# Kernel tuning notes

Hardware: AMD Instinct MI355X
Metric: run time of the kernel (lower is better)

Reference implementation:

```python
import jax, jax.numpy as jnp
import numpy as np

N_NODES = 100000
DIM = 64
N_EDGES = 1250000
PRESERVE = 0.1  # preserve_ratio in GCN module


def gcn_conv(x, W, b, row, col, edge_w, num_nodes):
    """PyG GCNConv with normalize=True: symmetric norm with added self-loops.
    x: [N, d], W: [d, d_out], edge (row -> col) with weight edge_w: [E].
    """
    # add self-loops with weight 1
    loop = jnp.arange(num_nodes, dtype=row.dtype)
    r = jnp.concatenate([row, loop])
    c = jnp.concatenate([col, loop])
    w = jnp.concatenate([edge_w, jnp.ones((num_nodes,), dtype=edge_w.dtype)])
    # symmetric degree normalization: deg computed at target (col)
    deg = jax.ops.segment_sum(w, c, num_segments=num_nodes)
    dinv = jnp.where(deg > 0, jax.lax.rsqrt(deg), 0.0)
    norm = dinv[r] * w * dinv[c]  # [E+N]
    xw = x @ W  # [N, d_out] (linear transform before propagation)
    msg = xw[r] * norm[:, None]  # gather + scale
    out = jax.ops.segment_sum(msg, c, num_segments=num_nodes)  # scatter-add at targets
    return out + b


def setup_inputs() -> dict:
    key = jax.random.key(0)
    ks = jax.random.split(key, 8)
    skill_embed = jax.random.normal(ks[0], (N_NODES, DIM), dtype=jnp.float32)
    edge_index = jax.random.randint(ks[1], (2, N_EDGES), 0, N_NODES, dtype=jnp.int64)
    edge_attr = jax.random.uniform(ks[2], (N_EDGES,), dtype=jnp.float32)
    # GCNConv params (W stored as [in, out] here), glorot-ish init
    scale = 1.0 / np.sqrt(DIM)
    W1 = jax.random.uniform(ks[3], (DIM, DIM), minval=-scale, maxval=scale, dtype=jnp.float32)
    b1 = jnp.zeros((DIM,), dtype=jnp.float32)
    W2 = jax.random.uniform(ks[4], (DIM, DIM), minval=-scale, maxval=scale, dtype=jnp.float32)
    b2 = jnp.zeros((DIM,), dtype=jnp.float32)
    return {"skill_embed": skill_embed, "edge_index": edge_index, "edge_attr": edge_attr,
            "W1": W1, "b1": b1, "W2": W2, "b2": b2}


def reference(skill_embed, edge_index, edge_attr, W1, b1, W2, b2):
    row, col = edge_index[0], edge_index[1]
    n = skill_embed.shape[0]
    temp = skill_embed
    out = gcn_conv(skill_embed, W1, b1, row, col, edge_attr, n)
    temp = (1.0 - PRESERVE) * out + PRESERVE * temp
    out = gcn_conv(temp, W2, b2, row, col, edge_attr, n)
    temp = (1.0 - PRESERVE) * out + PRESERVE * temp
    return temp
```

## Files before the change

### kernel.cpp

```cpp
#include <hip/hip_runtime.h>

#define DIM 64
#define PRESERVE 0.1f

typedef unsigned short bf16_t;

__device__ __forceinline__ float readlane_f(float v, int l) {
    return __int_as_float(__builtin_amdgcn_readlane(__float_as_int(v), l));
}
__device__ __forceinline__ float bf2f(bf16_t u) {
    return __uint_as_float(((unsigned)u) << 16);
}
__device__ __forceinline__ bf16_t f2bf(float f) {
    unsigned u = __float_as_uint(f);
    unsigned r = (u + 0x7FFFu + ((u >> 16) & 1u)) >> 16;
    return (bf16_t)r;
}

__global__ void k_init(int* cursor, int n) {
    int i = blockIdx.x * blockDim.x + threadIdx.x;
    if (i < n) cursor[i] = 0;
}

__global__ void k_hist4(const int4* __restrict__ col4, int* cursor,
                        int4* __restrict__ rank4, int nthreads) {
    int t = blockIdx.x * blockDim.x + threadIdx.x;
    if (t >= nthreads) return;
    int4 c = col4[t];
    int4 r;
    r.x = atomicAdd(&cursor[c.x], 1);
    r.y = atomicAdd(&cursor[c.y], 1);
    r.z = atomicAdd(&cursor[c.z], 1);
    r.w = atomicAdd(&cursor[c.w], 1);
    rank4[t] = r;
}

__global__ void k_hist1(const int* __restrict__ col, int* cursor,
                        int* __restrict__ rank, int E) {
    int e = blockIdx.x * blockDim.x + threadIdx.x;
    if (e < E) rank[e] = atomicAdd(&cursor[col[e]], 1);
}

__global__ __launch_bounds__(256) void k_scan1(const int* __restrict__ counts,
                                               int* __restrict__ offsets,
                                               int* __restrict__ blksum, int n) {
    __shared__ int s[256];
    int t = threadIdx.x;
    int idx = blockIdx.x * 256 + t;
    int v = (idx < n) ? counts[idx] : 0;
    s[t] = v;
    __syncthreads();
    for (int off = 1; off < 256; off <<= 1) {
        int x = (t >= off) ? s[t - off] : 0;
        __syncthreads();
        s[t] += x;
        __syncthreads();
    }
    if (idx < n) offsets[idx] = s[t];
    if (t == 255) blksum[blockIdx.x] = s[255];
}

__global__ __launch_bounds__(512) void k_scan2(const int* __restrict__ blksum,
                                               int* __restrict__ blkoff, int nblk) {
    __shared__ int s[512];
    int t = threadIdx.x;
    int v = (t < nblk) ? blksum[t] : 0;
    s[t] = v;
    __syncthreads();
    for (int off = 1; off < 512; off <<= 1) {
        int x = (t >= off) ? s[t - off] : 0;
        __syncthreads();
        s[t] += x;
        __syncthreads();
    }
    if (t < nblk) blkoff[t] = s[t] - v;
}

__global__ __launch_bounds__(256) void k_scan3(const int* __restrict__ counts,
                                               int* __restrict__ offsets,
                                               const int* __restrict__ blkoff,
                                               int n, int E) {
    int t = threadIdx.x;
    int idx = blockIdx.x * 256 + t;
    if (idx < n) offsets[idx] = offsets[idx] - counts[idx] + blkoff[blockIdx.x];
    if (idx == 0) offsets[n] = E;
}

__global__ void k_fill4(const int4* __restrict__ row4, const int4* __restrict__ col4,
                        const float4* __restrict__ w4, const int4* __restrict__ rank4,
                        const int* __restrict__ offsets, int2* __restrict__ sedge,
                        int nthreads) {
    int t = blockIdx.x * blockDim.x + threadIdx.x;
    if (t >= nthreads) return;
    int4 r = row4[t];
    int4 c = col4[t];
    float4 w = w4[t];
    int4 k = rank4[t];
    int2 p;
    p.x = r.x; p.y = __float_as_int(w.x); sedge[offsets[c.x] + k.x] = p;
    p.x = r.y; p.y = __float_as_int(w.y); sedge[offsets[c.y] + k.y] = p;
    p.x = r.z; p.y = __float_as_int(w.z); sedge[offsets[c.z] + k.z] = p;
    p.x = r.w; p.y = __float_as_int(w.w); sedge[offsets[c.w] + k.w] = p;
}

__global__ void k_fill1(const int* __restrict__ row, const int* __restrict__ col,
                        const float* __restrict__ w, const int* __restrict__ rank,
                        const int* __restrict__ offsets, int2* __restrict__ sedge,
                        int E) {
    int e = blockIdx.x * blockDim.x + threadIdx.x;
    if (e >= E) return;
    int2 p;
    p.x = row[e];
    p.y = __float_as_int(w[e]);
    sedge[offsets[col[e]] + rank[e]] = p;
}

__global__ __launch_bounds__(256) void k_deg_seg(const int2* __restrict__ sedge,
                                                 const int* __restrict__ offsets,
                                                 float* __restrict__ dinv, int n) {
    int tid = threadIdx.x;
    int lane = tid & 63;
    int c = blockIdx.x * 4 + (tid >> 6);
    if (c >= n) return;
    int beg = offsets[c];
    int end = offsets[c + 1];
    float s = 0.0f;
    for (int j = beg + lane; j < end; j += 64) s += __int_as_float(sedge[j].y);
    for (int off = 32; off > 0; off >>= 1) s += __shfl_xor(s, off);
    if (lane == 0) {
        float d = 1.0f + s;
        dinv[c] = (d > 0.0f) ? rsqrtf(d) : 0.0f;
    }
}

__global__ __launch_bounds__(256) void k_mm(
        const float* __restrict__ x, const float* __restrict__ W,
        const float* __restrict__ dinv, bf16_t* __restrict__ xs, int n) {
    int tid = threadIdx.x;
    int lane = tid & 63;
    int waveId = blockIdx.x * 4 + (tid >> 6);
    int nWaves = gridDim.x * 4;

    float Wr[DIM];
#pragma unroll
    for (int k = 0; k < DIM; ++k) Wr[k] = W[k * DIM + lane];

    for (int r0 = waveId * 4; r0 < n; r0 += nWaves * 4) {
        if (r0 + 3 < n) {
            float x0 = x[(size_t)(r0 + 0) * DIM + lane];
            float x1 = x[(size_t)(r0 + 1) * DIM + lane];
            float x2 = x[(size_t)(r0 + 2) * DIM + lane];
            float x3 = x[(size_t)(r0 + 3) * DIM + lane];
            float a0 = 0.f, a1 = 0.f, a2 = 0.f, a3 = 0.f;
#pragma unroll
            for (int k = 0; k < DIM; ++k) {
                float w = Wr[k];
                a0 += readlane_f(x0, k) * w;
                a1 += readlane_f(x1, k) * w;
                a2 += readlane_f(x2, k) * w;
                a3 += readlane_f(x3, k) * w;
            }
            xs[(size_t)(r0 + 0) * DIM + lane] = f2bf(a0 * dinv[r0 + 0]);
            xs[(size_t)(r0 + 1) * DIM + lane] = f2bf(a1 * dinv[r0 + 1]);
            xs[(size_t)(r0 + 2) * DIM + lane] = f2bf(a2 * dinv[r0 + 2]);
            xs[(size_t)(r0 + 3) * DIM + lane] = f2bf(a3 * dinv[r0 + 3]);
        } else {
            for (int r = r0; r < n; ++r) {
                float xv = x[(size_t)r * DIM + lane];
                float a = 0.f;
#pragma unroll
                for (int k = 0; k < DIM; ++k) a += readlane_f(xv, k) * Wr[k];
                xs[(size_t)r * DIM + lane] = f2bf(a * dinv[r]);
            }
        }
    }
}

__global__ __launch_bounds__(256) void k_gather(
        const bf16_t* __restrict__ xs, const int* __restrict__ offsets,
        const int2* __restrict__ sedge, const float* __restrict__ dinv,
        const float* __restrict__ b, const float* __restrict__ xprev,
        float* __restrict__ out, int n) {
    int tid = threadIdx.x;
    int lane = tid & 63;
    int c = blockIdx.x * 4 + (tid >> 6);
    if (c >= n) return;
    float di = dinv[c];
    float acc = bf2f(xs[(size_t)c * DIM + lane]);
    int beg = offsets[c];
    int end = offsets[c + 1];
    for (int b0 = beg; b0 < end; b0 += 64) {
        int m = end - b0;
        if (m > 64) m = 64;
        int r_l = 0, w_l = 0;
        if (lane < m) {
            int2 p = sedge[b0 + lane];
            r_l = p.x;
            w_l = p.y;
        }
        int j = 0;
        for (; j + 3 < m; j += 4) {
            int r0 = __builtin_amdgcn_readlane(r_l, j);
            int r1 = __builtin_amdgcn_readlane(r_l, j + 1);
            int r2 = __builtin_amdgcn_readlane(r_l, j + 2);
            int r3 = __builtin_amdgcn_readlane(r_l, j + 3);
            float w0 = readlane_f(__int_as_float(w_l), j);
            float w1 = readlane_f(__int_as_float(w_l), j + 1);
            float w2 = readlane_f(__int_as_float(w_l), j + 2);
            float w3 = readlane_f(__int_as_float(w_l), j + 3);
            float a0 = bf2f(xs[(size_t)r0 * DIM + lane]);
            float a1 = bf2f(xs[(size_t)r1 * DIM + lane]);
            float a2 = bf2f(xs[(size_t)r2 * DIM + lane]);
            float a3 = bf2f(xs[(size_t)r3 * DIM + lane]);
            acc += a0 * w0;
            acc += a1 * w1;
            acc += a2 * w2;
            acc += a3 * w3;
        }
        for (; j < m; ++j) {
            int r0 = __builtin_amdgcn_readlane(r_l, j);
            float w0 = readlane_f(__int_as_float(w_l), j);
            acc += bf2f(xs[(size_t)r0 * DIM + lane]) * w0;
        }
    }
    float v = (1.0f - PRESERVE) * (acc * di + b[lane]) + PRESERVE * xprev[(size_t)c * DIM + lane];
    out[(size_t)c * DIM + lane] = v;
}

extern "C" void kernel_launch(void* const* d_in, const int* in_sizes, int n_in,
                              void* d_out, int out_size, void* d_ws, size_t ws_size,
                              hipStream_t stream) {
    const float* x  = (const float*)d_in[0];
    const int*   ei = (const int*)d_in[1];
    const float* ew = (const float*)d_in[2];
    const float* W1 = (const float*)d_in[3];
    const float* b1 = (const float*)d_in[4];
    const float* W2 = (const float*)d_in[5];
    const float* b2 = (const float*)d_in[6];

    const int N = in_sizes[0] / DIM;
    const int E = in_sizes[2];
    const int* row = ei;
    const int* col = ei + E;

    int2* sedge   = (int2*)d_ws;
    float* dinv   = (float*)(sedge + E);
    float* temp   = dinv + N;
    bf16_t* xs    = (bf16_t*)(temp + (size_t)N * DIM);
    int* rank     = (int*)(xs + (size_t)N * DIM);
    int* cursor   = rank + E;
    int* offsets  = cursor + N;
    int* blksum   = offsets + N + 1;
    int* blkoff   = blksum + 640;

    const int B = 256;
    const int nblkN = (N + B - 1) / B;
    const int nblkG = (N + 3) / 4;
    const int nblkMM = 1024;

    k_init<<<nblkN, B, 0, stream>>>(cursor, N);

    if ((E & 3) == 0) {
        int nt = E / 4;
        k_hist4<<<(nt + B - 1) / B, B, 0, stream>>>((const int4*)col, cursor, (int4*)rank, nt);
    } else {
        k_hist1<<<(E + B - 1) / B, B, 0, stream>>>(col, cursor, rank, E);
    }

    k_scan1<<<nblkN, B, 0, stream>>>(cursor, offsets, blksum, N);
    k_scan2<<<1, 512, 0, stream>>>(blksum, blkoff, nblkN);
    k_scan3<<<nblkN, B, 0, stream>>>(cursor, offsets, blkoff, N, E);

    if ((E & 3) == 0) {
        int nt = E / 4;
        k_fill4<<<(nt + B - 1) / B, B, 0, stream>>>((const int4*)row, (const int4*)col,
                                                    (const float4*)ew, (const int4*)rank,
                                                    offsets, sedge, nt);
    } else {
        k_fill1<<<(E + B - 1) / B, B, 0, stream>>>(row, col, ew, rank, offsets, sedge, E);
    }

    k_deg_seg<<<nblkG, B, 0, stream>>>(sedge, offsets, dinv, N);

    k_mm<<<nblkMM, B, 0, stream>>>(x, W1, dinv, xs, N);
    k_gather<<<nblkG, B, 0, stream>>>(xs, offsets, sedge, dinv, b1, x, temp, N);

    k_mm<<<nblkMM, B, 0, stream>>>(temp, W2, dinv, xs, N);
    k_gather<<<nblkG, B, 0, stream>>>(xs, offsets, sedge, dinv, b2, temp, (float*)d_out, N);
}
```

Before: 333.0 us.

## Fuse first matmul into histogram kernel and second matmul into first gather

The first X·W1 transform no longer depends on dinv, so it runs inside the histogram launch, with one third of the blocks doing atomics and the rest doing the matmul. The source-side dinv factor is folded into the edge weights by a new rescale pass. The second matmul is fused into the first gather's epilogue through a persistent-wave loop, removing a separate launch and a round trip of temp. The cost is one extra pass over the edges and a fixed 1/3 block split that may leave work unbalanced. xs2 shares memory with rank, which is only safe because rank is no longer needed by the time xs2 is written.

```diff
diff --git a/kernel.cpp b/kernel.cpp
--- a/kernel.cpp
+++ b/kernel.cpp
@@ -22,23 +22,71 @@
     if (i < n) cursor[i] = 0;
 }
 
-__global__ void k_hist4(const int4* __restrict__ col4, int* cursor,
-                        int4* __restrict__ rank4, int nthreads) {
-    int t = blockIdx.x * blockDim.x + threadIdx.x;
-    if (t >= nthreads) return;
-    int4 c = col4[t];
-    int4 r;
-    r.x = atomicAdd(&cursor[c.x], 1);
-    r.y = atomicAdd(&cursor[c.y], 1);
-    r.z = atomicAdd(&cursor[c.z], 1);
-    r.w = atomicAdd(&cursor[c.w], 1);
-    rank4[t] = r;
-}
-
-__global__ void k_hist1(const int* __restrict__ col, int* cursor,
-                        int* __restrict__ rank, int E) {
-    int e = blockIdx.x * blockDim.x + threadIdx.x;
-    if (e < E) rank[e] = atomicAdd(&cursor[col[e]], 1);
+__global__ __launch_bounds__(256) void k_hist_mm(
+        const int* __restrict__ col, int* __restrict__ cursor,
+        int* __restrict__ rank, int E,
+        const float* __restrict__ x, const float* __restrict__ W,
+        bf16_t* __restrict__ xs, int n) {
+    int bid = blockIdx.x;
+    int G = gridDim.x;
+    if (bid % 3 == 0) {
+        int hb = bid / 3;
+        int nhb = (G + 2) / 3;
+        int tid0 = hb * 256 + threadIdx.x;
+        int nthreads = nhb * 256;
+        int nvec = E >> 2;
+        const int4* col4 = (const int4*)col;
+        int4* rank4 = (int4*)rank;
+        for (int t = tid0; t < nvec; t += nthreads) {
+            int4 c = col4[t];
+            int4 r;
+            r.x = atomicAdd(&cursor[c.x], 1);
+            r.y = atomicAdd(&cursor[c.y], 1);
+            r.z = atomicAdd(&cursor[c.z], 1);
+            r.w = atomicAdd(&cursor[c.w], 1);
+            rank4[t] = r;
+        }
+        for (int e = (nvec << 2) + tid0; e < E; e += nthreads)
+            rank[e] = atomicAdd(&cursor[col[e]], 1);
+    } else {
+        int mb = bid - (bid / 3) - 1;
+        int nmb = G - (G + 2) / 3;
+        int lane = threadIdx.x & 63;
+        int waveId = mb * 4 + (threadIdx.x >> 6);
+        int nWaves = nmb * 4;
+        float Wr[DIM];
+#pragma unroll
+        for (int k = 0; k < DIM; ++k) Wr[k] = W[k * DIM + lane];
+        for (int r0 = waveId * 4; r0 < n; r0 += nWaves * 4) {
+            if (r0 + 3 < n) {
+                float x0 = x[(size_t)(r0 + 0) * DIM + lane];
+                float x1 = x[(size_t)(r0 + 1) * DIM + lane];
+                float x2 = x[(size_t)(r0 + 2) * DIM + lane];
+                float x3 = x[(size_t)(r0 + 3) * DIM + lane];
+                float a0 = 0.f, a1 = 0.f, a2 = 0.f, a3 = 0.f;
+#pragma unroll
+                for (int k = 0; k < DIM; ++k) {
+                    float w = Wr[k];
+                    a0 += readlane_f(x0, k) * w;
+                    a1 += readlane_f(x1, k) * w;
+                    a2 += readlane_f(x2, k) * w;
+                    a3 += readlane_f(x3, k) * w;
+                }
+                xs[(size_t)(r0 + 0) * DIM + lane] = f2bf(a0);
+                xs[(size_t)(r0 + 1) * DIM + lane] = f2bf(a1);
+                xs[(size_t)(r0 + 2) * DIM + lane] = f2bf(a2);
+                xs[(size_t)(r0 + 3) * DIM + lane] = f2bf(a3);
+            } else {
+                for (int r = r0; r < n; ++r) {
+                    float xv = x[(size_t)r * DIM + lane];
+                    float a = 0.f;
+#pragma unroll
+                    for (int k = 0; k < DIM; ++k) a += readlane_f(xv, k) * Wr[k];
+                    xs[(size_t)r * DIM + lane] = f2bf(a);
+                }
+            }
+        }
+    }
 }
 
 __global__ __launch_bounds__(256) void k_scan1(const int* __restrict__ counts,
@@ -133,60 +181,83 @@
     }
 }
 
-__global__ __launch_bounds__(256) void k_mm(
-        const float* __restrict__ x, const float* __restrict__ W,
-        const float* __restrict__ dinv, bf16_t* __restrict__ xs, int n) {
-    int tid = threadIdx.x;
-    int lane = tid & 63;
-    int waveId = blockIdx.x * 4 + (tid >> 6);
+__global__ void k_rescale(int2* sedge, const float* __restrict__ dinv, int E) {
+    int e = blockIdx.x * blockDim.x + threadIdx.x;
+    if (e >= E) return;
+    int2 p = sedge[e];
+    p.y = __float_as_int(__int_as_float(p.y) * dinv[p.x]);
+    sedge[e] = p;
+}
+
+__global__ __launch_bounds__(256) void k_gather_mm(
+        const bf16_t* __restrict__ xs1, const int* __restrict__ offsets,
+        const int2* __restrict__ sedge, const float* __restrict__ dinv,
+        const float* __restrict__ b, const float* __restrict__ xprev,
+        const float* __restrict__ W2, float* __restrict__ temp,
+        bf16_t* __restrict__ xs2, int n) {
+    int lane = threadIdx.x & 63;
+    int waveId = blockIdx.x * 4 + (threadIdx.x >> 6);
     int nWaves = gridDim.x * 4;
 
-    float Wr[DIM];
-#pragma unroll
-    for (int k = 0; k < DIM; ++k) Wr[k] = W[k * DIM + lane];
-
-    for (int r0 = waveId * 4; r0 < n; r0 += nWaves * 4) {
-        if (r0 + 3 < n) {
-            float x0 = x[(size_t)(r0 + 0) * DIM + lane];
-            float x1 = x[(size_t)(r0 + 1) * DIM + lane];
-            float x2 = x[(size_t)(r0 + 2) * DIM + lane];
-            float x3 = x[(size_t)(r0 + 3) * DIM + lane];
-            float a0 = 0.f, a1 = 0.f, a2 = 0.f, a3 = 0.f;
-#pragma unroll
-            for (int k = 0; k < DIM; ++k) {
-                float w = Wr[k];
-                a0 += readlane_f(x0, k) * w;
-                a1 += readlane_f(x1, k) * w;
-                a2 += readlane_f(x2, k) * w;
-                a3 += readlane_f(x3, k) * w;
+    float W2r[DIM];
+#pragma unroll
+    for (int k = 0; k < DIM; ++k) W2r[k] = W2[k * DIM + lane];
+
+    for (int c = waveId; c < n; c += nWaves) {
+        float di = dinv[c];
+        float acc = di * bf2f(xs1[(size_t)c * DIM + lane]);
+        int beg = offsets[c];
+        int end = offsets[c + 1];
+        for (int b0 = beg; b0 < end; b0 += 64) {
+            int m = end - b0;
+            if (m > 64) m = 64;
+            int r_l = 0, w_l = 0;
+            if (lane < m) {
+                int2 p = sedge[b0 + lane];
+                r_l = p.x;
+                w_l = p.y;
             }
-            xs[(size_t)(r0 + 0) * DIM + lane] = f2bf(a0 * dinv[r0 + 0]);
-            xs[(size_t)(r0 + 1) * DIM + lane] = f2bf(a1 * dinv[r0 + 1]);
-            xs[(size_t)(r0 + 2) * DIM + lane] = f2bf(a2 * dinv[r0 + 2]);
-            xs[(size_t)(r0 + 3) * DIM + lane] = f2bf(a3 * dinv[r0 + 3]);
-        } else {
-            for (int r = r0; r < n; ++r) {
-                float xv = x[(size_t)r * DIM + lane];
-                float a = 0.f;
-#pragma unroll
-                for (int k = 0; k < DIM; ++k) a += readlane_f(xv, k) * Wr[k];
-                xs[(size_t)r * DIM + lane] = f2bf(a * dinv[r]);
+            int j = 0;
+            for (; j + 3 < m; j += 4) {
+                int r0 = __builtin_amdgcn_readlane(r_l, j);
+                int r1 = __builtin_amdgcn_readlane(r_l, j + 1);
+                int r2 = __builtin_amdgcn_readlane(r_l, j + 2);
+                int r3 = __builtin_amdgcn_readlane(r_l, j + 3);
+                float w0 = readlane_f(__int_as_float(w_l), j);
+                float w1 = readlane_f(__int_as_float(w_l), j + 1);
+                float w2 = readlane_f(__int_as_float(w_l), j + 2);
+                float w3 = readlane_f(__int_as_float(w_l), j + 3);
+                acc += bf2f(xs1[(size_t)r0 * DIM + lane]) * w0;
+                acc += bf2f(xs1[(size_t)r1 * DIM + lane]) * w1;
+                acc += bf2f(xs1[(size_t)r2 * DIM + lane]) * w2;
+                acc += bf2f(xs1[(size_t)r3 * DIM + lane]) * w3;
             }
-        }
-    }
-}
-
-__global__ __launch_bounds__(256) void k_gather(
-        const bf16_t* __restrict__ xs, const int* __restrict__ offsets,
+            for (; j < m; ++j) {
+                int r0 = __builtin_amdgcn_readlane(r_l, j);
+                float w0 = readlane_f(__int_as_float(w_l), j);
+                acc += bf2f(xs1[(size_t)r0 * DIM + lane]) * w0;
+            }
+        }
+        float tv = (1.0f - PRESERVE) * (acc * di + b[lane])
+                 + PRESERVE * xprev[(size_t)c * DIM + lane];
+        temp[(size_t)c * DIM + lane] = tv;
+        float a = 0.f;
+#pragma unroll
+        for (int k = 0; k < DIM; ++k) a += readlane_f(tv, k) * W2r[k];
+        xs2[(size_t)c * DIM + lane] = f2bf(a);
+    }
+}
+
+__global__ __launch_bounds__(256) void k_gather2(
+        const bf16_t* __restrict__ xs2, const int* __restrict__ offsets,
         const int2* __restrict__ sedge, const float* __restrict__ dinv,
         const float* __restrict__ b, const float* __restrict__ xprev,
         float* __restrict__ out, int n) {
-    int tid = threadIdx.x;
-    int lane = tid & 63;
-    int c = blockIdx.x * 4 + (tid >> 6);
+    int lane = threadIdx.x & 63;
+    int c = blockIdx.x * 4 + (threadIdx.x >> 6);
     if (c >= n) return;
     float di = dinv[c];
-    float acc = bf2f(xs[(size_t)c * DIM + lane]);
+    float acc = di * bf2f(xs2[(size_t)c * DIM + lane]);
     int beg = offsets[c];
     int end = offsets[c + 1];
     for (int b0 = beg; b0 < end; b0 += 64) {
@@ -208,22 +279,19 @@
             float w1 = readlane_f(__int_as_float(w_l), j + 1);
             float w2 = readlane_f(__int_as_float(w_l), j + 2);
             float w3 = readlane_f(__int_as_float(w_l), j + 3);
-            float a0 = bf2f(xs[(size_t)r0 * DIM + lane]);
-            float a1 = bf2f(xs[(size_t)r1 * DIM + lane]);
-            float a2 = bf2f(xs[(size_t)r2 * DIM + lane]);
-            float a3 = bf2f(xs[(size_t)r3 * DIM + lane]);
-            acc += a0 * w0;
-            acc += a1 * w1;
-            acc += a2 * w2;
-            acc += a3 * w3;
+            acc += bf2f(xs2[(size_t)r0 * DIM + lane]) * w0;
+            acc += bf2f(xs2[(size_t)r1 * DIM + lane]) * w1;
+            acc += bf2f(xs2[(size_t)r2 * DIM + lane]) * w2;
+            acc += bf2f(xs2[(size_t)r3 * DIM + lane]) * w3;
         }
         for (; j < m; ++j) {
             int r0 = __builtin_amdgcn_readlane(r_l, j);
             float w0 = readlane_f(__int_as_float(w_l), j);
-            acc += bf2f(xs[(size_t)r0 * DIM + lane]) * w0;
-        }
-    }
-    float v = (1.0f - PRESERVE) * (acc * di + b[lane]) + PRESERVE * xprev[(size_t)c * DIM + lane];
+            acc += bf2f(xs2[(size_t)r0 * DIM + lane]) * w0;
+        }
+    }
+    float v = (1.0f - PRESERVE) * (acc * di + b[lane])
+            + PRESERVE * xprev[(size_t)c * DIM + lane];
     out[(size_t)c * DIM + lane] = v;
 }
 
@@ -246,26 +314,23 @@
     int2* sedge   = (int2*)d_ws;
     float* dinv   = (float*)(sedge + E);
     float* temp   = dinv + N;
-    bf16_t* xs    = (bf16_t*)(temp + (size_t)N * DIM);
-    int* rank     = (int*)(xs + (size_t)N * DIM);
+    bf16_t* xs1   = (bf16_t*)(temp + (size_t)N * DIM);
+    bf16_t* xs2   = xs1 + (size_t)N * DIM;
+    int* rank     = (int*)xs2;
     int* cursor   = rank + E;
-    int* offsets  = cursor + N;
+    int* offsets  = (int*)(xs2 + (size_t)N * DIM);
     int* blksum   = offsets + N + 1;
     int* blkoff   = blksum + 640;
 
     const int B = 256;
     const int nblkN = (N + B - 1) / B;
     const int nblkG = (N + 3) / 4;
-    const int nblkMM = 1024;
+    const int G2 = 1536;
+    const int nblkGM = 1024;
 
     k_init<<<nblkN, B, 0, stream>>>(cursor, N);
 
-    if ((E & 3) == 0) {
-        int nt = E / 4;
-        k_hist4<<<(nt + B - 1) / B, B, 0, stream>>>((const int4*)col, cursor, (int4*)rank, nt);
-    } else {
-        k_hist1<<<(E + B - 1) / B, B, 0, stream>>>(col, cursor, rank, E);
-    }
+    k_hist_mm<<<G2, B, 0, stream>>>(col, cursor, rank, E, x, W1, xs1, N);
 
     k_scan1<<<nblkN, B, 0, stream>>>(cursor, offsets, blksum, N);
     k_scan2<<<1, 512, 0, stream>>>(blksum, blkoff, nblkN);
@@ -281,10 +346,10 @@
     }
 
     k_deg_seg<<<nblkG, B, 0, stream>>>(sedge, offsets, dinv, N);
-
-    k_mm<<<nblkMM, B, 0, stream>>>(x, W1, dinv, xs, N);
-    k_gather<<<nblkG, B, 0, stream>>>(xs, offsets, sedge, dinv, b1, x, temp, N);
-
-    k_mm<<<nblkMM, B, 0, stream>>>(temp, W2, dinv, xs, N);
-    k_gather<<<nblkG, B, 0, stream>>>(xs, offsets, sedge, dinv, b2, temp, (float*)d_out, N);
-}
+    k_rescale<<<(E + B - 1) / B, B, 0, stream>>>(sedge, dinv, E);
+
+    k_gather_mm<<<nblkGM, B, 0, stream>>>(xs1, offsets, sedge, dinv, b1, x,
+                                          W2, temp, xs2, N);
+    k_gather2<<<nblkG, B, 0, stream>>>(xs2, offsets, sedge, dinv, b2, temp,
+                                       (float*)d_out, N);
+}
```

Result: slower. 345.9 us (+3.9%).

## Overlap histogram with first matmul, use decoupled-lookback scan, fuse degree scaling

Applied to the files above, without the earlier changes.

The edge-target histogram and the first layer's x@W1 now run in one kernel, with a third of the blocks doing atomics and the rest doing the matmul, so the atomic-bound and compute-bound work share the machine. The three-pass scan is replaced by a single-pass chunked scan that chains chunks through per-chunk status flags, and the cursor clear becomes a memset. Degree normalisation scaling and the bf16 conversion of the first layer's features are fused into the degree kernel. This removes several launches but adds a spin-wait between scan blocks and an extra full-precision intermediate write and read.

```diff
diff --git a/kernel.cpp b/kernel.cpp
--- a/kernel.cpp
+++ b/kernel.cpp
@@ -2,6 +2,7 @@
 
 #define DIM 64
 #define PRESERVE 0.1f
+#define SCHUNK 1024
 
 typedef unsigned short bf16_t;
 
@@ -17,73 +18,134 @@
     return (bf16_t)r;
 }
 
-__global__ void k_init(int* cursor, int n) {
-    int i = blockIdx.x * blockDim.x + threadIdx.x;
-    if (i < n) cursor[i] = 0;
-}
-
-__global__ void k_hist4(const int4* __restrict__ col4, int* cursor,
-                        int4* __restrict__ rank4, int nthreads) {
-    int t = blockIdx.x * blockDim.x + threadIdx.x;
-    if (t >= nthreads) return;
-    int4 c = col4[t];
-    int4 r;
-    r.x = atomicAdd(&cursor[c.x], 1);
-    r.y = atomicAdd(&cursor[c.y], 1);
-    r.z = atomicAdd(&cursor[c.z], 1);
-    r.w = atomicAdd(&cursor[c.w], 1);
-    rank4[t] = r;
-}
-
-__global__ void k_hist1(const int* __restrict__ col, int* cursor,
-                        int* __restrict__ rank, int E) {
-    int e = blockIdx.x * blockDim.x + threadIdx.x;
-    if (e < E) rank[e] = atomicAdd(&cursor[col[e]], 1);
-}
-
-__global__ __launch_bounds__(256) void k_scan1(const int* __restrict__ counts,
-                                               int* __restrict__ offsets,
-                                               int* __restrict__ blksum, int n) {
+__global__ __launch_bounds__(256) void k_hist_mm(
+        const int* __restrict__ col, int* __restrict__ cursor,
+        int* __restrict__ rank, int E,
+        const float* __restrict__ x, const float* __restrict__ W,
+        float* __restrict__ temp, int n) {
+    const int G = gridDim.x;
+    const int Gh = G / 3;
+    const int bid = blockIdx.x;
+    const int tid = threadIdx.x;
+    if (bid < Gh) {
+        int t0 = bid * 256 + tid;
+        int nh = Gh * 256;
+        int nvec = E >> 2;
+        const int4* col4 = (const int4*)col;
+        int4* rank4 = (int4*)rank;
+        for (int t = t0; t < nvec; t += nh) {
+            int4 c = col4[t];
+            int4 r;
+            r.x = atomicAdd(&cursor[c.x], 1);
+            r.y = atomicAdd(&cursor[c.y], 1);
+            r.z = atomicAdd(&cursor[c.z], 1);
+            r.w = atomicAdd(&cursor[c.w], 1);
+            rank4[t] = r;
+        }
+        for (int e = (nvec << 2) + t0; e < E; e += nh)
+            rank[e] = atomicAdd(&cursor[col[e]], 1);
+    } else {
+        int mb = bid - Gh;
+        int nmb = G - Gh;
+        int lane = tid & 63;
+        int waveId = mb * 4 + (tid >> 6);
+        int nWaves = nmb * 4;
+        float Wr[DIM];
+#pragma unroll
+        for (int k = 0; k < DIM; ++k) Wr[k] = W[k * DIM + lane];
+        for (int r0 = waveId * 4; r0 < n; r0 += nWaves * 4) {
+            if (r0 + 3 < n) {
+                float x0 = x[(size_t)(r0 + 0) * DIM + lane];
+                float x1 = x[(size_t)(r0 + 1) * DIM + lane];
+                float x2 = x[(size_t)(r0 + 2) * DIM + lane];
+                float x3 = x[(size_t)(r0 + 3) * DIM + lane];
+                float a0 = 0.f, a1 = 0.f, a2 = 0.f, a3 = 0.f;
+#pragma unroll
+                for (int k = 0; k < DIM; ++k) {
+                    float w = Wr[k];
+                    a0 += readlane_f(x0, k) * w;
+                    a1 += readlane_f(x1, k) * w;
+                    a2 += readlane_f(x2, k) * w;
+                    a3 += readlane_f(x3, k) * w;
+                }
+                temp[(size_t)(r0 + 0) * DIM + lane] = a0;
+                temp[(size_t)(r0 + 1) * DIM + lane] = a1;
+                temp[(size_t)(r0 + 2) * DIM + lane] = a2;
+                temp[(size_t)(r0 + 3) * DIM + lane] = a3;
+            } else {
+                for (int r = r0; r < n; ++r) {
+                    float xv = x[(size_t)r * DIM + lane];
+                    float a = 0.f;
+#pragma unroll
+                    for (int k = 0; k < DIM; ++k) a += readlane_f(xv, k) * Wr[k];
+                    temp[(size_t)r * DIM + lane] = a;
+                }
+            }
+        }
+    }
+}
+
+__global__ __launch_bounds__(256) void k_scan_lb(
+        const int* __restrict__ cursor, int* __restrict__ offsets,
+        unsigned int* __restrict__ state, int N, int E, int nch) {
     __shared__ int s[256];
-    int t = threadIdx.x;
-    int idx = blockIdx.x * 256 + t;
-    int v = (idx < n) ? counts[idx] : 0;
-    s[t] = v;
+    __shared__ int s_run;
+    const int ch = blockIdx.x;
+    const int tid = threadIdx.x;
+    const int base = ch * SCHUNK + tid * 4;
+
+    int a0 = 0, a1 = 0, a2 = 0, a3 = 0;
+    if (base + 3 < N) {
+        int4 v = *(const int4*)(cursor + base);
+        a0 = v.x; a1 = v.y; a2 = v.z; a3 = v.w;
+    } else {
+        if (base < N) a0 = cursor[base];
+        if (base + 1 < N) a1 = cursor[base + 1];
+        if (base + 2 < N) a2 = cursor[base + 2];
+        if (base + 3 < N) a3 = cursor[base + 3];
+    }
+    int ts = a0 + a1 + a2 + a3;
+    s[tid] = ts;
     __syncthreads();
     for (int off = 1; off < 256; off <<= 1) {
-        int x = (t >= off) ? s[t - off] : 0;
+        int xv = (tid >= off) ? s[tid - off] : 0;
         __syncthreads();
-        s[t] += x;
+        s[tid] += xv;
         __syncthreads();
     }
-    if (idx < n) offsets[idx] = s[t];
-    if (t == 255) blksum[blockIdx.x] = s[255];
-}
-
-__global__ __launch_bounds__(512) void k_scan2(const int* __restrict__ blksum,
-                                               int* __restrict__ blkoff, int nblk) {
-    __shared__ int s[512];
-    int t = threadIdx.x;
-    int v = (t < nblk) ? blksum[t] : 0;
-    s[t] = v;
+    int excl_thr = s[tid] - ts;
+    int total = s[255];
+
+    if (tid == 0) {
+        if (ch == 0) {
+            __hip_atomic_store(&state[0], (2u << 30) | (unsigned)total,
+                               __ATOMIC_RELEASE, __HIP_MEMORY_SCOPE_AGENT);
+            s_run = 0;
+        } else {
+            __hip_atomic_store(&state[ch], (1u << 30) | (unsigned)total,
+                               __ATOMIC_RELEASE, __HIP_MEMORY_SCOPE_AGENT);
+            int running = 0;
+            for (int j = ch - 1; j >= 0; --j) {
+                unsigned st;
+                do {
+                    st = __hip_atomic_load(&state[j], __ATOMIC_ACQUIRE,
+                                           __HIP_MEMORY_SCOPE_AGENT);
+                } while ((st >> 30) == 0u);
+                running += (int)(st & ((1u << 30) - 1u));
+                if ((st >> 30) == 2u) break;
+            }
+            __hip_atomic_store(&state[ch], (2u << 30) | (unsigned)(running + total),
+                               __ATOMIC_RELEASE, __HIP_MEMORY_SCOPE_AGENT);
+            s_run = running;
+        }
+    }
     __syncthreads();
-    for (int off = 1; off < 512; off <<= 1) {
-        int x = (t >= off) ? s[t - off] : 0;
-        __syncthreads();
-        s[t] += x;
-        __syncthreads();
-    }
-    if (t < nblk) blkoff[t] = s[t] - v;
-}
-
-__global__ __launch_bounds__(256) void k_scan3(const int* __restrict__ counts,
-                                               int* __restrict__ offsets,
-                                               const int* __restrict__ blkoff,
-                                               int n, int E) {
-    int t = threadIdx.x;
-    int idx = blockIdx.x * 256 + t;
-    if (idx < n) offsets[idx] = offsets[idx] - counts[idx] + blkoff[blockIdx.x];
-    if (idx == 0) offsets[n] = E;
+    int e = s_run + excl_thr;
+    if (base < N) offsets[base] = e;
+    if (base + 1 < N) offsets[base + 1] = e + a0;
+    if (base + 2 < N) offsets[base + 2] = e + a0 + a1;
+    if (base + 3 < N) offsets[base + 3] = e + a0 + a1 + a2;
+    if (ch == nch - 1 && tid == 0) offsets[N] = E;
 }
 
 __global__ void k_fill4(const int4* __restrict__ row4, const int4* __restrict__ col4,
@@ -115,9 +177,10 @@
     sedge[offsets[col[e]] + rank[e]] = p;
 }
 
-__global__ __launch_bounds__(256) void k_deg_seg(const int2* __restrict__ sedge,
-                                                 const int* __restrict__ offsets,
-                                                 float* __restrict__ dinv, int n) {
+__global__ __launch_bounds__(256) void k_deg_scale(
+        const int2* __restrict__ sedge, const int* __restrict__ offsets,
+        const float* __restrict__ temp, float* __restrict__ dinv,
+        bf16_t* __restrict__ xs1, int n) {
     int tid = threadIdx.x;
     int lane = tid & 63;
     int c = blockIdx.x * 4 + (tid >> 6);
@@ -127,10 +190,10 @@
     float s = 0.0f;
     for (int j = beg + lane; j < end; j += 64) s += __int_as_float(sedge[j].y);
     for (int off = 32; off > 0; off >>= 1) s += __shfl_xor(s, off);
-    if (lane == 0) {
-        float d = 1.0f + s;
-        dinv[c] = (d > 0.0f) ? rsqrtf(d) : 0.0f;
-    }
+    float d = 1.0f + s;
+    float di = (d > 0.0f) ? rsqrtf(d) : 0.0f;
+    if (lane == 0) dinv[c] = di;
+    xs1[(size_t)c * DIM + lane] = f2bf(temp[(size_t)c * DIM + lane] * di);
 }
 
 __global__ __launch_bounds__(256) void k_mm(
@@ -181,9 +244,8 @@
         const int2* __restrict__ sedge, const float* __restrict__ dinv,
         const float* __restrict__ b, const float* __restrict__ xprev,
         float* __restrict__ out, int n) {
-    int tid = threadIdx.x;
-    int lane = tid & 63;
-    int c = blockIdx.x * 4 + (tid >> 6);
+    int lane = threadIdx.x & 63;
+    int c = blockIdx.x * 4 + (threadIdx.x >> 6);
     if (c >= n) return;
     float di = dinv[c];
     float acc = bf2f(xs[(size_t)c * DIM + lane]);
@@ -208,14 +270,10 @@
             float w1 = readlane_f(__int_as_float(w_l), j + 1);
             float w2 = readlane_f(__int_as_float(w_l), j + 2);
             float w3 = readlane_f(__int_as_float(w_l), j + 3);
-            float a0 = bf2f(xs[(size_t)r0 * DIM + lane]);
-            float a1 = bf2f(xs[(size_t)r1 * DIM + lane]);
-            float a2 = bf2f(xs[(size_t)r2 * DIM + lane]);
-            float a3 = bf2f(xs[(size_t)r3 * DIM + lane]);
-            acc += a0 * w0;
-            acc += a1 * w1;
-            acc += a2 * w2;
-            acc += a3 * w3;
+            acc += bf2f(xs[(size_t)r0 * DIM + lane]) * w0;
+            acc += bf2f(xs[(size_t)r1 * DIM + lane]) * w1;
+            acc += bf2f(xs[(size_t)r2 * DIM + lane]) * w2;
+            acc += bf2f(xs[(size_t)r3 * DIM + lane]) * w3;
         }
         for (; j < m; ++j) {
             int r0 = __builtin_amdgcn_readlane(r_l, j);
@@ -223,7 +281,8 @@
             acc += bf2f(xs[(size_t)r0 * DIM + lane]) * w0;
         }
     }
-    float v = (1.0f - PRESERVE) * (acc * di + b[lane]) + PRESERVE * xprev[(size_t)c * DIM + lane];
+    float v = (1.0f - PRESERVE) * (acc * di + b[lane])
+            + PRESERVE * xprev[(size_t)c * DIM + lane];
     out[(size_t)c * DIM + lane] = v;
 }
 
@@ -243,33 +302,28 @@
     const int* row = ei;
     const int* col = ei + E;
 
+    const int nch = (N + SCHUNK - 1) / SCHUNK;
+
     int2* sedge   = (int2*)d_ws;
     float* dinv   = (float*)(sedge + E);
     float* temp   = dinv + N;
-    bf16_t* xs    = (bf16_t*)(temp + (size_t)N * DIM);
-    int* rank     = (int*)(xs + (size_t)N * DIM);
+    bf16_t* xs1   = (bf16_t*)(temp + (size_t)N * DIM);
+    bf16_t* xs2   = xs1 + (size_t)N * DIM;
+    int* rank     = (int*)(xs2 + (size_t)N * DIM);
     int* cursor   = rank + E;
-    int* offsets  = cursor + N;
-    int* blksum   = offsets + N + 1;
-    int* blkoff   = blksum + 640;
+    unsigned int* state = (unsigned int*)(cursor + N);
+    int* offsets  = (int*)(state + 128);
 
     const int B = 256;
-    const int nblkN = (N + B - 1) / B;
     const int nblkG = (N + 3) / 4;
+    const int G_HM = 1536;
     const int nblkMM = 1024;
 
-    k_init<<<nblkN, B, 0, stream>>>(cursor, N);
-
-    if ((E & 3) == 0) {
-        int nt = E / 4;
-        k_hist4<<<(nt + B - 1) / B, B, 0, stream>>>((const int4*)col, cursor, (int4*)rank, nt);
-    } else {
-        k_hist1<<<(E + B - 1) / B, B, 0, stream>>>(col, cursor, rank, E);
-    }
-
-    k_scan1<<<nblkN, B, 0, stream>>>(cursor, offsets, blksum, N);
-    k_scan2<<<1, 512, 0, stream>>>(blksum, blkoff, nblkN);
-    k_scan3<<<nblkN, B, 0, stream>>>(cursor, offsets, blkoff, N, E);
+    hipMemsetAsync(cursor, 0, (size_t)(N + 128) * sizeof(int), stream);
+
+    k_hist_mm<<<G_HM, B, 0, stream>>>(col, cursor, rank, E, x, W1, temp, N);
+
+    k_scan_lb<<<nch, B, 0, stream>>>(cursor, offsets, state, N, E, nch);
 
     if ((E & 3) == 0) {
         int nt = E / 4;
@@ -280,11 +334,10 @@
         k_fill1<<<(E + B - 1) / B, B, 0, stream>>>(row, col, ew, rank, offsets, sedge, E);
     }
 
-    k_deg_seg<<<nblkG, B, 0, stream>>>(sedge, offsets, dinv, N);
-
-    k_mm<<<nblkMM, B, 0, stream>>>(x, W1, dinv, xs, N);
-    k_gather<<<nblkG, B, 0, stream>>>(xs, offsets, sedge, dinv, b1, x, temp, N);
-
-    k_mm<<<nblkMM, B, 0, stream>>>(temp, W2, dinv, xs, N);
-    k_gather<<<nblkG, B, 0, stream>>>(xs, offsets, sedge, dinv, b2, temp, (float*)d_out, N);
-}
+    k_deg_scale<<<nblkG, B, 0, stream>>>(sedge, offsets, temp, dinv, xs1, N);
+
+    k_gather<<<nblkG, B, 0, stream>>>(xs1, offsets, sedge, dinv, b1, x, temp, N);
+    k_mm<<<nblkMM, B, 0, stream>>>(temp, W2, dinv, xs2, N);
+    k_gather<<<nblkG, B, 0, stream>>>(xs2, offsets, sedge, dinv, b2, temp,
+                                      (float*)d_out, N);
+}
```

Measured after the change: 356.3 us. 1.07x slower.
